# Kernel optimization log

Hardware: AMD Instinct MI355X
Metric: run time of the kernel (lower is better)

The kernel has to match this reference:

```python
import jax, jax.numpy as jnp
import numpy as np

# Geometry constants (equidistant flat-detector fan beam)
B, A, D = 16, 1024, 1024      # batch, n_projections, detector bins
H, W = 512, 512               # reconstruction grid
VX = 1.0                      # pixel spacing (mm)
DU = 1.25                     # detector bin spacing (mm)
D_SI = 750.0                  # source-isocenter distance (mm)
D_SD = 1200.0                 # source-detector distance (mm)


def setup_inputs() -> dict:
    key = jax.random.key(0)
    sino = jax.random.normal(key, (B, A, D), dtype=jnp.float32)
    # Ram-Lak ramp filter in FFT ordering (matches torch.fft.fft bin layout)
    filt = jnp.asarray(np.abs(np.fft.fftfreq(D)).astype(np.float32))
    angles = jnp.asarray(np.linspace(0.0, 2.0 * np.pi, A, endpoint=False).astype(np.float32))
    return {"sinogram": sino, "filt": filt, "angles": angles}


def _backproject(fsino, angles):
    # fsino: [B, A, D] filtered sinogram -> image [B, H, W]
    xs = (jnp.arange(W, dtype=jnp.float32) - (W - 1) / 2.0) * VX
    ys = (jnp.arange(H, dtype=jnp.float32) - (H - 1) / 2.0) * VX
    X, Y = jnp.meshgrid(xs, ys, indexing="xy")  # [H, W] world coords (mm)

    def body(acc, inp):
        beta, proj = inp  # beta scalar, proj [B, D]
        c, s = jnp.cos(beta), jnp.sin(beta)
        t = D_SI + X * c + Y * s            # distance from source along central ray [H,W]
        u = D_SD * (-X * s + Y * c) / t     # detector coordinate (mm) [H,W]
        idx = u / DU + (D - 1) / 2.0        # fractional detector index
        i0 = jnp.clip(jnp.floor(idx), 0, D - 2).astype(jnp.int32)
        frac = jnp.clip(idx - i0.astype(jnp.float32), 0.0, 1.0)
        inside = (idx >= 0.0) & (idx <= D - 1.0)
        v0 = jnp.take(proj, i0, axis=1)       # [B, H, W]
        v1 = jnp.take(proj, i0 + 1, axis=1)   # [B, H, W]
        val = v0 * (1.0 - frac) + v1 * frac
        w = (D_SI / t) ** 2                   # fan-beam distance weighting
        acc = acc + jnp.where(inside, val * w, 0.0)
        return acc, None

    acc0 = jnp.zeros((B, H, W), jnp.float32)
    acc, _ = jax.lax.scan(body, acc0, (angles, jnp.swapaxes(fsino, 0, 1)))
    return acc * (jnp.pi / A)  # angular integration step


def reference(sinogram, filt, angles):
    # FFT ramp filtering along detector axis (ortho norm, as in torch code)
    f = jnp.fft.fft(sinogram, axis=-1, norm="ortho")
    f = f * filt
    x = jnp.fft.ifft(f, axis=-1, norm="ortho").real.astype(jnp.float32)
    return _backproject(x, angles)
```

## Files before the change

### kernel.cpp

```cpp
#include <hip/hip_runtime.h>
#include <hip/hip_fp16.h>
#include <math.h>

#define N_B 16
#define N_A 1024
#define N_D 1024
#define N_H 512
#define N_W 512

typedef _Float16 half2t __attribute__((ext_vector_type(2)));

__device__ inline half2t h2cast(unsigned u) {
    union { unsigned u; half2t h; } cv; cv.u = u; return cv.h;
}

__device__ inline float fdot2f(half2t a, half2t b, float c) {
#if __has_builtin(__builtin_amdgcn_fdot2)
    return __builtin_amdgcn_fdot2(a, b, c, false);
#else
    asm("v_dot2_f32_f16 %0, %1, %2, %0" : "+v"(c) : "v"(a), "v"(b));
    return c;
#endif
}

__device__ inline half2t pack_h2(float lo, float hi) {
#if __has_builtin(__builtin_amdgcn_cvt_pkrtz)
    auto r = __builtin_amdgcn_cvt_pkrtz(lo, hi);
    union { decltype(r) a; half2t h; } cv; cv.a = r; return cv.h;
#else
    half2t r; r.x = (_Float16)lo; r.y = (_Float16)hi; return r;
#endif
}

__device__ inline unsigned pack_u(float lo, float hi) {
    union { half2t h; unsigned u; } cv; cv.h = pack_h2(lo, hi); return cv.u;
}

__device__ inline float med3f(float a, float lo, float hi) {
#if __has_builtin(__builtin_amdgcn_fmed3f)
    return __builtin_amdgcn_fmed3f(a, lo, hi);
#else
    return fminf(fmaxf(a, lo), hi);
#endif
}

__global__ void fan_setup_kernel(const float* __restrict__ angles,
                                 float* __restrict__ twr,
                                 float* __restrict__ twi,
                                 float2* __restrict__ cs) {
    int t = blockIdx.x * 256 + threadIdx.x;
    if (t < 512) {
        double ang = -2.0 * M_PI * (double)t / 1024.0;
        twr[t] = (float)cos(ang);
        twi[t] = (float)sin(ang);
    }
    if (t < 1024) {
        double b = (double)angles[t];
        cs[t] = make_float2((float)cos(b), (float)sin(b));
    }
}

__global__ __launch_bounds__(256) void fan_umin_kernel(
    const float2* __restrict__ cs, unsigned* __restrict__ utab) {
    const int t = blockIdx.x * 256 + threadIdx.x;
    const int a = t & (N_A - 1);
    const int tile = t >> 10;
    const float2 p = cs[a];
    const float c = p.x, s = p.y;
    const float x0 = (float)((tile & 15) * 32) - 255.5f;
    const float x1 = x0 + 31.0f;
    const float y0 = (float)((tile >> 4) * 32) - 255.5f;
    const float y1 = y0 + 31.0f;
    float m = 1e30f;
#pragma unroll
    for (int i = 0; i < 4; ++i) {
        const float xx = (i & 1) ? x1 : x0;
        const float yy = (i & 2) ? y1 : y0;
        const float tt = 750.0f + xx * c + yy * s;
        const float idx = (960.0f * (yy * c - xx * s)) / tt + 511.5f;
        m = fminf(m, idx);
    }
    int base = (int)floorf(m) - 2;
    base = base < 0 ? 0 : (base > 768 ? 768 : base);
    utab[t] = (unsigned)base;
}

__global__ __launch_bounds__(256) void fan_fft_filter4_kernel(
    const float* __restrict__ sino, const float* __restrict__ filt,
    const float* __restrict__ twr_g, const float* __restrict__ twi_g,
    uint4* __restrict__ pf4) {
    __shared__ float s_re0[1024], s_im0[1024];
    __shared__ float s_re1[1024], s_im1[1024];
    __shared__ float s_twr[512], s_twi[512];

    const int tid = threadIdx.x;
    const int a = blockIdx.x & (N_A - 1);
    const int g = blockIdx.x >> 10;

    {
        float2 t0 = ((const float2*)twr_g)[tid];
        s_twr[2 * tid] = t0.x; s_twr[2 * tid + 1] = t0.y;
        float2 t1 = ((const float2*)twi_g)[tid];
        s_twi[2 * tid] = t1.x; s_twi[2 * tid + 1] = t1.y;
    }
    {
        const size_t rowstride = (size_t)N_A * N_D;
        const float* rb = sino + (size_t)(4 * g) * rowstride + (size_t)a * N_D;
        ((float4*)s_re0)[tid] = ((const float4*)(rb + 0 * rowstride))[tid];
        ((float4*)s_im0)[tid] = ((const float4*)(rb + 1 * rowstride))[tid];
        ((float4*)s_re1)[tid] = ((const float4*)(rb + 2 * rowstride))[tid];
        ((float4*)s_im1)[tid] = ((const float4*)(rb + 3 * rowstride))[tid];
    }
    __syncthreads();

    for (int L = 9; L >= 0; --L) {
        const int half = 1 << L;
#pragma unroll
        for (int q = 0; q < 4; ++q) {
            float* re = (q < 2) ? s_re0 : s_re1;
            float* im = (q < 2) ? s_im0 : s_im1;
            const int bf = tid + ((q & 1) << 8);
            const int j = bf & (half - 1);
            const int blk = bf >> L;
            const int base = (blk << (L + 1)) + j;
            const int tw = j << (9 - L);
            const float wr = s_twr[tw], wi = s_twi[tw];
            const float ar = re[base], ai = im[base];
            const float br = re[base + half], bi = im[base + half];
            re[base] = ar + br;
            im[base] = ai + bi;
            const float dr = ar - br, di = ai - bi;
            re[base + half] = dr * wr - di * wi;
            im[base + half] = dr * wi + di * wr;
        }
        __syncthreads();
    }

#pragma unroll
    for (int q = 0; q < 4; ++q) {
        const int i = tid + (q << 8);
        const int ri = (int)(__brev((unsigned)i) >> 22);
        const float f = filt[ri];
        s_re0[i] *= f; s_im0[i] *= f;
        s_re1[i] *= f; s_im1[i] *= f;
    }
    __syncthreads();

    for (int L = 0; L <= 9; ++L) {
        const int half = 1 << L;
#pragma unroll
        for (int q = 0; q < 4; ++q) {
            float* re = (q < 2) ? s_re0 : s_re1;
            float* im = (q < 2) ? s_im0 : s_im1;
            const int bf = tid + ((q & 1) << 8);
            const int j = bf & (half - 1);
            const int blk = bf >> L;
            const int base = (blk << (L + 1)) + j;
            const int tw = j << (9 - L);
            const float wr = s_twr[tw], wi = -s_twi[tw];
            const float ar = re[base], ai = im[base];
            const float tr = re[base + half], ti = im[base + half];
            const float br = tr * wr - ti * wi;
            const float bi = tr * wi + ti * wr;
            re[base] = ar + br;
            im[base] = ai + bi;
            re[base + half] = ar - br;
            im[base + half] = ai - bi;
        }
        __syncthreads();
    }

    const float invN = 1.0f / 1024.0f;
    uint4* dst = pf4 + ((size_t)g * N_A + (size_t)a) * N_D;
#pragma unroll
    for (int q = 0; q < 4; ++q) {
        const int n = tid + (q << 8);
        const int n1 = (n < 1023) ? n + 1 : n;
        const float e = (n < 1023) ? 1.0f : 0.0f;
        uint4 v;
        v.x = pack_u(s_re0[n] * invN, s_re0[n1] * invN * e);
        v.y = pack_u(s_im0[n] * invN, s_im0[n1] * invN * e);
        v.z = pack_u(s_re1[n] * invN, s_re1[n1] * invN * e);
        v.w = pack_u(s_im1[n] * invN, s_im1[n1] * invN * e);
        dst[n] = v;
    }
}

#define ABODY(WB, K_, PF_)                                                    \
    {                                                                         \
        const int k_ = (K_);                                                  \
        (WB)[tid] = pre;                                                      \
        if (PF_) {                                                            \
            const unsigned e_ = s_ub[k_ + 1] + se;                            \
            pre = gsrc[(((unsigned)(abase + k_ + 1)) << 10) + e_];            \
        }                                                                     \
        __syncthreads();                                                      \
        const float2 csp = lcs[k_];                                           \
        const float c = csp.x, s = csp.y;                                     \
        const unsigned ub = s_ub[k_];                                         \
        const unsigned abk = ((unsigned)(abase + k_)) << 10;                  \
        const float t0v = fmaf(x, c, fmaf(y0, s, 750.0f));                    \
        const float num0 = fmaf(y0, c, -(x * s));                             \
        const float t1v = fmaf(16.0f, s, t0v);                                \
        const float num1 = fmaf(16.0f, c, num0);                              \
        const float r0 = __builtin_amdgcn_rcpf(t0v);                          \
        const float r1 = __builtin_amdgcn_rcpf(t1v);                          \
        const float idxA = fmaf(num0 * r0, 960.0f, 511.5f);                   \
        const float idxB = fmaf(num1 * r1, 960.0f, 511.5f);                   \
        const float idxcA = med3f(idxA, 0.0f, 1023.0f);                       \
        const float idxcB = med3f(idxB, 0.0f, 1023.0f);                       \
        const float i0fA = floorf(idxcA);                                     \
        const float i0fB = floorf(idxcB);                                     \
        const float frA = idxcA - i0fA;                                       \
        const float frB = idxcB - i0fB;                                       \
        const float waA = 750.0f * r0, waB = 750.0f * r1;                     \
        float wdA = waA * waA, wdB = waB * waB;                               \
        wdA = (idxA == idxcA) ? wdA : 0.0f;                                   \
        wdB = (idxB == idxcB) ? wdB : 0.0f;                                   \
        const float w1A = wdA * frA, w1B = wdB * frB;                         \
        const half2t wpA = pack_h2(wdA - w1A, w1A);                           \
        const half2t wpB = pack_h2(wdB - w1B, w1B);                           \
        const int i0A = (int)i0fA, i0B = (int)i0fB;                           \
        const unsigned offA = abk + (unsigned)i0A;                            \
        const unsigned offB = abk + (unsigned)i0B;                            \
        const unsigned oiA = ((unsigned)(i0A - (int)ub)) & 255u;              \
        const unsigned oiB = ((unsigned)(i0B - (int)ub)) & 255u;              \
        const uint4 a0 = g0[offA];                                            \
        const uint4 a1 = g1[offA];                                            \
        const uint4 a2 = (WB)[oiA];                                           \
        const uint4 a3 = (WB)[256u + oiA];                                    \
        const uint4 b0 = g0[offB];                                            \
        const uint4 b1 = g1[offB];                                            \
        const uint4 b2 = (WB)[oiB];                                           \
        const uint4 b3 = (WB)[256u + oiB];                                    \
        acc0[0] = fdot2f(h2cast(a0.x), wpA, acc0[0]);                         \
        acc0[1] = fdot2f(h2cast(a0.y), wpA, acc0[1]);                         \
        acc0[2] = fdot2f(h2cast(a0.z), wpA, acc0[2]);                         \
        acc0[3] = fdot2f(h2cast(a0.w), wpA, acc0[3]);                         \
        acc0[4] = fdot2f(h2cast(a1.x), wpA, acc0[4]);                         \
        acc0[5] = fdot2f(h2cast(a1.y), wpA, acc0[5]);                         \
        acc0[6] = fdot2f(h2cast(a1.z), wpA, acc0[6]);                         \
        acc0[7] = fdot2f(h2cast(a1.w), wpA, acc0[7]);                         \
        acc0[8] = fdot2f(h2cast(a2.x), wpA, acc0[8]);                         \
        acc0[9] = fdot2f(h2cast(a2.y), wpA, acc0[9]);                         \
        acc0[10] = fdot2f(h2cast(a2.z), wpA, acc0[10]);                       \
        acc0[11] = fdot2f(h2cast(a2.w), wpA, acc0[11]);                       \
        acc0[12] = fdot2f(h2cast(a3.x), wpA, acc0[12]);                       \
        acc0[13] = fdot2f(h2cast(a3.y), wpA, acc0[13]);                       \
        acc0[14] = fdot2f(h2cast(a3.z), wpA, acc0[14]);                       \
        acc0[15] = fdot2f(h2cast(a3.w), wpA, acc0[15]);                       \
        acc1[0] = fdot2f(h2cast(b0.x), wpB, acc1[0]);                         \
        acc1[1] = fdot2f(h2cast(b0.y), wpB, acc1[1]);                         \
        acc1[2] = fdot2f(h2cast(b0.z), wpB, acc1[2]);                         \
        acc1[3] = fdot2f(h2cast(b0.w), wpB, acc1[3]);                         \
        acc1[4] = fdot2f(h2cast(b1.x), wpB, acc1[4]);                         \
        acc1[5] = fdot2f(h2cast(b1.y), wpB, acc1[5]);                         \
        acc1[6] = fdot2f(h2cast(b1.z), wpB, acc1[6]);                         \
        acc1[7] = fdot2f(h2cast(b1.w), wpB, acc1[7]);                         \
        acc1[8] = fdot2f(h2cast(b2.x), wpB, acc1[8]);                         \
        acc1[9] = fdot2f(h2cast(b2.y), wpB, acc1[9]);                         \
        acc1[10] = fdot2f(h2cast(b2.z), wpB, acc1[10]);                       \
        acc1[11] = fdot2f(h2cast(b2.w), wpB, acc1[11]);                       \
        acc1[12] = fdot2f(h2cast(b3.x), wpB, acc1[12]);                       \
        acc1[13] = fdot2f(h2cast(b3.y), wpB, acc1[13]);                       \
        acc1[14] = fdot2f(h2cast(b3.z), wpB, acc1[14]);                       \
        acc1[15] = fdot2f(h2cast(b3.w), wpB, acc1[15]);                       \
    }

template <int SPLIT>
__global__ __launch_bounds__(512, 4) void fan_backproject_kernel(
    const uint4* __restrict__ pf4, const float2* __restrict__ cs_g,
    const unsigned* __restrict__ utab, float* __restrict__ dst0) {
    constexpr int ACNT = N_A / SPLIT;
    __shared__ float2 lcs[ACNT];
    __shared__ unsigned s_ub[ACNT];
    __shared__ uint4 win[2][512];
    const int tid = threadIdx.x;

    int part, tile;
    if (SPLIT == 4) {
        part = blockIdx.x & 3;
        tile = blockIdx.x >> 2;
    } else {
        part = 0;
        tile = blockIdx.x;
    }
    const int abase = part * ACNT;

    const unsigned* __restrict__ utrow = utab + (size_t)tile * N_A + abase;
    for (int i = tid; i < ACNT; i += 512) {
        lcs[i] = cs_g[abase + i];
        s_ub[i] = utrow[i];
    }

    const int xi = (tile & 15) * 32 + (tid & 31);
    const int yi0 = (tile >> 4) * 32 + (tid >> 5);
    const float x = (float)xi - 255.5f;
    const float y0 = (float)yi0 - 255.5f;

    const uint4* __restrict__ g0 = pf4;
    const uint4* __restrict__ g1 = pf4 + ((size_t)1 << 20);
    const unsigned sg = (unsigned)tid >> 8;
    const unsigned se = (unsigned)tid & 255u;
    const uint4* __restrict__ gsrc = pf4 + ((size_t)(2 + sg) << 20);

    float acc0[N_B], acc1[N_B];
#pragma unroll
    for (int b = 0; b < N_B; ++b) { acc0[b] = 0.0f; acc1[b] = 0.0f; }

    uint4* wb0 = &win[0][0];
    uint4* wb1 = &win[1][0];

    __syncthreads();

    uint4 pre;
    {
        const unsigned e = s_ub[0] + se;
        pre = gsrc[(((unsigned)abase) << 10) + e];
    }

    for (int kk = 0; kk + 2 < ACNT; kk += 2) {
        ABODY(wb0, kk, true);
        ABODY(wb1, kk + 1, true);
    }
    ABODY(wb0, ACNT - 2, true);
    ABODY(wb1, ACNT - 1, false);

    const float scale = 3.14159265358979323846f / 1024.0f;
    float* dst = dst0 + (size_t)part * ((size_t)N_B * N_H * N_W);
    const size_t pix0 = (size_t)yi0 * N_W + (size_t)xi;
    const size_t pix1 = pix0 + (size_t)16 * N_W;
#pragma unroll
    for (int b = 0; b < N_B; ++b) {
        dst[(size_t)b * (N_H * N_W) + pix0] = acc0[b] * scale;
        dst[(size_t)b * (N_H * N_W) + pix1] = acc1[b] * scale;
    }
}

template <int NS>
__global__ __launch_bounds__(256) void fan_reduce_kernel(
    const float4* __restrict__ p, float4* __restrict__ o) {
    const int i = blockIdx.x * 256 + threadIdx.x;
    const size_t stride = (size_t)N_B * N_H * N_W / 4;
    float4 v = p[i];
#pragma unroll
    for (int k = 1; k < NS; ++k) {
        const float4 w = p[(size_t)k * stride + i];
        v.x += w.x; v.y += w.y; v.z += w.z; v.w += w.w;
    }
    o[i] = v;
}

extern "C" void kernel_launch(void* const* d_in, const int* in_sizes, int n_in,
                              void* d_out, int out_size, void* d_ws, size_t ws_size,
                              hipStream_t stream) {
    const float* sino = (const float*)d_in[0];
    const float* filt = (const float*)d_in[1];
    const float* angles = (const float*)d_in[2];
    float* out = (float*)d_out;

    float* twr = (float*)d_ws;
    float* twi = twr + 512;
    float2* cs = (float2*)(twi + 512);
    char* base = (char*)d_ws;
    unsigned* utab = (unsigned*)(base + 16384);
    uint4* pf4 = (uint4*)(base + 16384 + (1 << 20));
    const size_t PF_BYTES = (size_t)4 * N_A * N_D * 16;
    float* partials = (float*)(base + 16384 + (1 << 20) + PF_BYTES);
    const size_t PART = (size_t)N_B * N_H * N_W;
    const size_t need4 = 16384 + (1 << 20) + PF_BYTES + 4 * PART * 4;
    const size_t need1 = 16384 + (1 << 20) + PF_BYTES;

    fan_setup_kernel<<<4, 256, 0, stream>>>(angles, twr, twi, cs);
    fan_umin_kernel<<<1024, 256, 0, stream>>>(cs, utab);
    fan_fft_filter4_kernel<<<4 * N_A, 256, 0, stream>>>(sino, filt, twr, twi,
                                                        pf4);
    if (ws_size >= need4) {
        fan_backproject_kernel<4><<<256 * 4, 512, 0, stream>>>(pf4, cs, utab,
                                                               partials);
        fan_reduce_kernel<4><<<(int)(PART / 4 / 256), 256, 0, stream>>>(
            (const float4*)partials, (float4*)out);
    } else if (ws_size >= need1) {
        fan_backproject_kernel<1><<<256, 512, 0, stream>>>(pf4, cs, utab,
                                                           out);
    }
}
```

Measured before the change: 485.2 us.

## Halve backprojection block size and compute four pixels per thread

```diff
diff --git a/kernel.cpp b/kernel.cpp
--- a/kernel.cpp
+++ b/kernel.cpp
@@ -186,89 +186,73 @@
     }
 }
 
+#define PIXEL(ACC, TV, NUMV, WB, ABK, UB)                                     \
+    {                                                                         \
+        const float r_ = __builtin_amdgcn_rcpf(TV);                           \
+        const float idx = fmaf((NUMV) * r_, 960.0f, 511.5f);                  \
+        const float idxc = med3f(idx, 0.0f, 1023.0f);                         \
+        const float i0f = floorf(idxc);                                       \
+        const float fr = idxc - i0f;                                          \
+        const float wa = 750.0f * r_;                                         \
+        float wd = wa * wa;                                                   \
+        wd = (idx == idxc) ? wd : 0.0f;                                       \
+        const float w1 = wd * fr;                                             \
+        const half2t wp = pack_h2(wd - w1, w1);                               \
+        const int i0 = (int)i0f;                                              \
+        const unsigned off = (ABK) + (unsigned)i0;                            \
+        const unsigned oi = ((unsigned)(i0 - (int)(UB))) & 255u;              \
+        const uint4 v0 = g0[off];                                             \
+        const uint4 v1 = g1[off];                                             \
+        const uint4 v2 = (WB)[oi];                                            \
+        const uint4 v3 = (WB)[256u + oi];                                     \
+        ACC[0] = fdot2f(h2cast(v0.x), wp, ACC[0]);                            \
+        ACC[1] = fdot2f(h2cast(v0.y), wp, ACC[1]);                            \
+        ACC[2] = fdot2f(h2cast(v0.z), wp, ACC[2]);                            \
+        ACC[3] = fdot2f(h2cast(v0.w), wp, ACC[3]);                            \
+        ACC[4] = fdot2f(h2cast(v1.x), wp, ACC[4]);                            \
+        ACC[5] = fdot2f(h2cast(v1.y), wp, ACC[5]);                            \
+        ACC[6] = fdot2f(h2cast(v1.z), wp, ACC[6]);                            \
+        ACC[7] = fdot2f(h2cast(v1.w), wp, ACC[7]);                            \
+        ACC[8] = fdot2f(h2cast(v2.x), wp, ACC[8]);                            \
+        ACC[9] = fdot2f(h2cast(v2.y), wp, ACC[9]);                            \
+        ACC[10] = fdot2f(h2cast(v2.z), wp, ACC[10]);                          \
+        ACC[11] = fdot2f(h2cast(v2.w), wp, ACC[11]);                          \
+        ACC[12] = fdot2f(h2cast(v3.x), wp, ACC[12]);                          \
+        ACC[13] = fdot2f(h2cast(v3.y), wp, ACC[13]);                          \
+        ACC[14] = fdot2f(h2cast(v3.z), wp, ACC[14]);                          \
+        ACC[15] = fdot2f(h2cast(v3.w), wp, ACC[15]);                          \
+    }
+
 #define ABODY(WB, K_, PF_)                                                    \
     {                                                                         \
         const int k_ = (K_);                                                  \
-        (WB)[tid] = pre;                                                      \
+        (WB)[tid] = pre2;                                                     \
+        (WB)[256 + tid] = pre3;                                               \
         if (PF_) {                                                            \
-            const unsigned e_ = s_ub[k_ + 1] + se;                            \
-            pre = gsrc[(((unsigned)(abase + k_ + 1)) << 10) + e_];            \
+            const unsigned e_ = s_ub[k_ + 1] + (unsigned)tid;                 \
+            const unsigned ao_ = ((unsigned)(abase + k_ + 1)) << 10;          \
+            pre2 = gsrc2[ao_ + e_];                                           \
+            pre3 = gsrc3[ao_ + e_];                                           \
         }                                                                     \
         __syncthreads();                                                      \
         const float2 csp = lcs[k_];                                           \
         const float c = csp.x, s = csp.y;                                     \
         const unsigned ub = s_ub[k_];                                         \
         const unsigned abk = ((unsigned)(abase + k_)) << 10;                  \
-        const float t0v = fmaf(x, c, fmaf(y0, s, 750.0f));                    \
-        const float num0 = fmaf(y0, c, -(x * s));                             \
-        const float t1v = fmaf(16.0f, s, t0v);                                \
-        const float num1 = fmaf(16.0f, c, num0);                              \
-        const float r0 = __builtin_amdgcn_rcpf(t0v);                          \
-        const float r1 = __builtin_amdgcn_rcpf(t1v);                          \
-        const float idxA = fmaf(num0 * r0, 960.0f, 511.5f);                   \
-        const float idxB = fmaf(num1 * r1, 960.0f, 511.5f);                   \
-        const float idxcA = med3f(idxA, 0.0f, 1023.0f);                       \
-        const float idxcB = med3f(idxB, 0.0f, 1023.0f);                       \
-        const float i0fA = floorf(idxcA);                                     \
-        const float i0fB = floorf(idxcB);                                     \
-        const float frA = idxcA - i0fA;                                       \
-        const float frB = idxcB - i0fB;                                       \
-        const float waA = 750.0f * r0, waB = 750.0f * r1;                     \
-        float wdA = waA * waA, wdB = waB * waB;                               \
-        wdA = (idxA == idxcA) ? wdA : 0.0f;                                   \
-        wdB = (idxB == idxcB) ? wdB : 0.0f;                                   \
-        const float w1A = wdA * frA, w1B = wdB * frB;                         \
-        const half2t wpA = pack_h2(wdA - w1A, w1A);                           \
-        const half2t wpB = pack_h2(wdB - w1B, w1B);                           \
-        const int i0A = (int)i0fA, i0B = (int)i0fB;                           \
-        const unsigned offA = abk + (unsigned)i0A;                            \
-        const unsigned offB = abk + (unsigned)i0B;                            \
-        const unsigned oiA = ((unsigned)(i0A - (int)ub)) & 255u;              \
-        const unsigned oiB = ((unsigned)(i0B - (int)ub)) & 255u;              \
-        const uint4 a0 = g0[offA];                                            \
-        const uint4 a1 = g1[offA];                                            \
-        const uint4 a2 = (WB)[oiA];                                           \
-        const uint4 a3 = (WB)[256u + oiA];                                    \
-        const uint4 b0 = g0[offB];                                            \
-        const uint4 b1 = g1[offB];                                            \
-        const uint4 b2 = (WB)[oiB];                                           \
-        const uint4 b3 = (WB)[256u + oiB];                                    \
-        acc0[0] = fdot2f(h2cast(a0.x), wpA, acc0[0]);                         \
-        acc0[1] = fdot2f(h2cast(a0.y), wpA, acc0[1]);                         \
-        acc0[2] = fdot2f(h2cast(a0.z), wpA, acc0[2]);                         \
-        acc0[3] = fdot2f(h2cast(a0.w), wpA, acc0[3]);                         \
-        acc0[4] = fdot2f(h2cast(a1.x), wpA, acc0[4]);                         \
-        acc0[5] = fdot2f(h2cast(a1.y), wpA, acc0[5]);                         \
-        acc0[6] = fdot2f(h2cast(a1.z), wpA, acc0[6]);                         \
-        acc0[7] = fdot2f(h2cast(a1.w), wpA, acc0[7]);                         \
-        acc0[8] = fdot2f(h2cast(a2.x), wpA, acc0[8]);                         \
-        acc0[9] = fdot2f(h2cast(a2.y), wpA, acc0[9]);                         \
-        acc0[10] = fdot2f(h2cast(a2.z), wpA, acc0[10]);                       \
-        acc0[11] = fdot2f(h2cast(a2.w), wpA, acc0[11]);                       \
-        acc0[12] = fdot2f(h2cast(a3.x), wpA, acc0[12]);                       \
-        acc0[13] = fdot2f(h2cast(a3.y), wpA, acc0[13]);                       \
-        acc0[14] = fdot2f(h2cast(a3.z), wpA, acc0[14]);                       \
-        acc0[15] = fdot2f(h2cast(a3.w), wpA, acc0[15]);                       \
-        acc1[0] = fdot2f(h2cast(b0.x), wpB, acc1[0]);                         \
-        acc1[1] = fdot2f(h2cast(b0.y), wpB, acc1[1]);                         \
-        acc1[2] = fdot2f(h2cast(b0.z), wpB, acc1[2]);                         \
-        acc1[3] = fdot2f(h2cast(b0.w), wpB, acc1[3]);                         \
-        acc1[4] = fdot2f(h2cast(b1.x), wpB, acc1[4]);                         \
-        acc1[5] = fdot2f(h2cast(b1.y), wpB, acc1[5]);                         \
-        acc1[6] = fdot2f(h2cast(b1.z), wpB, acc1[6]);                         \
-        acc1[7] = fdot2f(h2cast(b1.w), wpB, acc1[7]);                         \
-        acc1[8] = fdot2f(h2cast(b2.x), wpB, acc1[8]);                         \
-        acc1[9] = fdot2f(h2cast(b2.y), wpB, acc1[9]);                         \
-        acc1[10] = fdot2f(h2cast(b2.z), wpB, acc1[10]);                       \
-        acc1[11] = fdot2f(h2cast(b2.w), wpB, acc1[11]);                       \
-        acc1[12] = fdot2f(h2cast(b3.x), wpB, acc1[12]);                       \
-        acc1[13] = fdot2f(h2cast(b3.y), wpB, acc1[13]);                       \
-        acc1[14] = fdot2f(h2cast(b3.z), wpB, acc1[14]);                       \
-        acc1[15] = fdot2f(h2cast(b3.w), wpB, acc1[15]);                       \
+        float tv = fmaf(x, c, fmaf(y0, s, 750.0f));                           \
+        float nv = fmaf(y0, c, -(x * s));                                     \
+        const float ds8 = 8.0f * s, dc8 = 8.0f * c;                           \
+        PIXEL(acc0, tv, nv, WB, abk, ub);                                     \
+        tv += ds8; nv += dc8;                                                 \
+        PIXEL(acc1, tv, nv, WB, abk, ub);                                     \
+        tv += ds8; nv += dc8;                                                 \
+        PIXEL(acc2, tv, nv, WB, abk, ub);                                     \
+        tv += ds8; nv += dc8;                                                 \
+        PIXEL(acc3, tv, nv, WB, abk, ub);                                     \
     }
 
 template <int SPLIT>
-__global__ __launch_bounds__(512, 4) void fan_backproject_kernel(
+__global__ __launch_bounds__(256, 4) void fan_backproject_kernel(
     const uint4* __restrict__ pf4, const float2* __restrict__ cs_g,
     const unsigned* __restrict__ utab, float* __restrict__ dst0) {
     constexpr int ACNT = N_A / SPLIT;
@@ -288,7 +272,7 @@
     const int abase = part * ACNT;
 
     const unsigned* __restrict__ utrow = utab + (size_t)tile * N_A + abase;
-    for (int i = tid; i < ACNT; i += 512) {
+    for (int i = tid; i < ACNT; i += 256) {
         lcs[i] = cs_g[abase + i];
         s_ub[i] = utrow[i];
     }
@@ -300,23 +284,26 @@
 
     const uint4* __restrict__ g0 = pf4;
     const uint4* __restrict__ g1 = pf4 + ((size_t)1 << 20);
-    const unsigned sg = (unsigned)tid >> 8;
-    const unsigned se = (unsigned)tid & 255u;
-    const uint4* __restrict__ gsrc = pf4 + ((size_t)(2 + sg) << 20);
-
-    float acc0[N_B], acc1[N_B];
-#pragma unroll
-    for (int b = 0; b < N_B; ++b) { acc0[b] = 0.0f; acc1[b] = 0.0f; }
+    const uint4* __restrict__ gsrc2 = pf4 + ((size_t)2 << 20);
+    const uint4* __restrict__ gsrc3 = pf4 + ((size_t)3 << 20);
+
+    float acc0[N_B], acc1[N_B], acc2[N_B], acc3[N_B];
+#pragma unroll
+    for (int b = 0; b < N_B; ++b) {
+        acc0[b] = 0.0f; acc1[b] = 0.0f; acc2[b] = 0.0f; acc3[b] = 0.0f;
+    }
 
     uint4* wb0 = &win[0][0];
     uint4* wb1 = &win[1][0];
 
     __syncthreads();
 
-    uint4 pre;
+    uint4 pre2, pre3;
     {
-        const unsigned e = s_ub[0] + se;
-        pre = gsrc[(((unsigned)abase) << 10) + e];
+        const unsigned e = s_ub[0] + (unsigned)tid;
+        const unsigned ao = ((unsigned)abase) << 10;
+        pre2 = gsrc2[ao + e];
+        pre3 = gsrc3[ao + e];
     }
 
     for (int kk = 0; kk + 2 < ACNT; kk += 2) {
@@ -329,11 +316,13 @@
     const float scale = 3.14159265358979323846f / 1024.0f;
     float* dst = dst0 + (size_t)part * ((size_t)N_B * N_H * N_W);
     const size_t pix0 = (size_t)yi0 * N_W + (size_t)xi;
-    const size_t pix1 = pix0 + (size_t)16 * N_W;
 #pragma unroll
     for (int b = 0; b < N_B; ++b) {
-        dst[(size_t)b * (N_H * N_W) + pix0] = acc0[b] * scale;
-        dst[(size_t)b * (N_H * N_W) + pix1] = acc1[b] * scale;
+        const size_t bo = (size_t)b * (N_H * N_W);
+        dst[bo + pix0] = acc0[b] * scale;
+        dst[bo + pix0 + (size_t)8 * N_W] = acc1[b] * scale;
+        dst[bo + pix0 + (size_t)16 * N_W] = acc2[b] * scale;
+        dst[bo + pix0 + (size_t)24 * N_W] = acc3[b] * scale;
     }
 }
 
@@ -376,12 +365,12 @@
     fan_fft_filter4_kernel<<<4 * N_A, 256, 0, stream>>>(sino, filt, twr, twi,
                                                         pf4);
     if (ws_size >= need4) {
-        fan_backproject_kernel<4><<<256 * 4, 512, 0, stream>>>(pf4, cs, utab,
+        fan_backproject_kernel<4><<<256 * 4, 256, 0, stream>>>(pf4, cs, utab,
                                                                partials);
         fan_reduce_kernel<4><<<(int)(PART / 4 / 256), 256, 0, stream>>>(
             (const float4*)partials, (float4*)out);
     } else if (ws_size >= need1) {
-        fan_backproject_kernel<1><<<256, 512, 0, stream>>>(pf4, cs, utab,
+        fan_backproject_kernel<1><<<256, 256, 0, stream>>>(pf4, cs, utab,
                                                            out);
     }
 }
```

Measured after the change: 722.5 us. +48.9%, slower.
